# Optimization experiments

Hardware: AMD Instinct MI355X
Metric: run time of the kernel (lower is better)

## Reference

```python
import jax, jax.numpy as jnp
import numpy as np

B, DIM, W = 16, 128, 16384
HEADS, DIM_HEAD = 4, 32
HIDDEN = HEADS * DIM_HEAD  # 128
SCALE = DIM_HEAD ** -0.5
EPS = 1e-5


def setup_inputs() -> dict:
    key = jax.random.key(0)
    k0, k1, k2, k3 = jax.random.split(key, 4)
    x = jax.random.normal(k0, (B, DIM, W), dtype=jnp.float32)
    # pointwise Conv1d weights (kernel_size=1) stored as [out_ch, in_ch]
    W_qkv = jax.random.normal(k1, (HIDDEN * 3, DIM), dtype=jnp.float32) * 0.02
    W_out = jax.random.normal(k2, (DIM, HIDDEN), dtype=jnp.float32) * 0.02
    b_out = jnp.zeros((DIM,), dtype=jnp.float32)
    gamma = jnp.ones((DIM,), dtype=jnp.float32)
    beta = jnp.zeros((DIM,), dtype=jnp.float32)
    return {"x": x, "W_qkv": W_qkv, "W_out": W_out, "b_out": b_out,
            "gamma": gamma, "beta": beta}


def reference(x, W_qkv, W_out, b_out, gamma, beta):
    b, c, w = x.shape
    # pointwise conv = channel matmul: (3*hidden, c) @ (b, c, w) -> (b, 3*hidden, w)
    qkv = jnp.einsum('oc,bcw->bow', W_qkv, x)
    q, k, v = jnp.split(qkv, 3, axis=1)
    rs = lambda t: t.reshape(b, HEADS, DIM_HEAD, w)  # b (h d) w -> b h d w
    q, k, v = rs(q), rs(k), rs(v)
    q = jax.nn.softmax(q, axis=-2) * SCALE   # softmax over head-dim d
    k = jax.nn.softmax(k, axis=-1)           # softmax over length n
    v = v / w
    # context: (b h d e) = sum_n k[b h d n] v[b h e n]
    context = jnp.einsum('bhdn,bhen->bhde', k, v)
    out = jnp.einsum('bhde,bhdn->bhen', context, q)  # (b h e n)
    out = out.reshape(b, HIDDEN, w)
    y = jnp.einsum('oc,bcw->bow', W_out, out) + b_out[None, :, None]
    # channel-wise LayerNorm over dim=1 (biased variance)
    mean = jnp.mean(y, axis=1, keepdims=True)
    var = jnp.var(y, axis=1, keepdims=True)
    y = (y - mean) * jax.lax.rsqrt(var + EPS)
    return y * gamma[None, :, None] + beta[None, :, None]
```

## Files before the change

### kernel.cpp

```cpp
#include <hip/hip_runtime.h>
#include <cstddef>

#define WLEN 16384
#define SCALEQ 0.17677669529663687f
#define CB_SCALE 16777216.0f
#define CB_INV   5.9604644775390625e-08f

typedef _Float16 half8 __attribute__((ext_vector_type(8)));
typedef _Float16 half4 __attribute__((ext_vector_type(4)));
typedef float float4v __attribute__((ext_vector_type(4)));

#define WS_CTX 0
#define WS_DEN 65536
#define WS_WH  67584
#define WS_CB  92160

#define MFMA16(a, b, c) __builtin_amdgcn_mfma_f32_16x16x32_f16(a, b, c, 0, 0, 0)

__global__ __launch_bounds__(256) void k0_prep(const float* __restrict__ Wqkv,
                                               float* __restrict__ ws) {
  int idx = blockIdx.x * 256 + threadIdx.x;
  _Float16* Wh = (_Float16*)(ws + WS_WH);
  if (idx < 49152) Wh[idx] = (_Float16)Wqkv[idx];
}

__global__ __launch_bounds__(256, 2) void ka_ctx(
    const float* __restrict__ x, float* __restrict__ ws) {
  __shared__ __align__(16) _Float16 xh[64 * 136];
  __shared__ __align__(16) _Float16 ekl[4][32 * 72];
  __shared__ __align__(16) _Float16 vl[4][32 * 72];
  const int tid = threadIdx.x;
  const int lane = tid & 63, wv = tid >> 6;
  const int l15 = lane & 15, quad = lane >> 4;
  const int b = blockIdx.y, chunk = blockIdx.x;
  const _Float16* Wh = (const _Float16*)(ws + WS_WH);
  float* ctx = ws + WS_CTX;
  float* den = ws + WS_DEN;
  const float* xb = x + (size_t)b * 128 * WLEN;

  half8 bw[4][4];
  #pragma unroll
  for (int nt = 0; nt < 4; ++nt) {
    int row = (nt < 2) ? (128 + 32 * wv + nt * 16 + l15)
                       : (256 + 32 * wv + (nt - 2) * 16 + l15);
    #pragma unroll
    for (int ks = 0; ks < 4; ++ks)
      bw[nt][ks] = *(const half8*)(Wh + row * 128 + ks * 32 + quad * 8);
  }

  const float4v zero4 = {0.f, 0.f, 0.f, 0.f};
  float4v ctxa[2][2] = {zero4, zero4, zero4, zero4};
  float denr[2] = {0.f, 0.f};
  const int f = tid & 7, cq = tid >> 3;

  for (int s = 0; s < 8; ++s) {
    const int n0 = chunk * 512 + s * 64;
    __syncthreads();
    #pragma unroll
    for (int it = 0; it < 2; ++it) {
      const int nn = it * 32 + 4 * f;
      const float* p = xb + (size_t)(4 * cq) * WLEN + n0 + nn;
      float4 r0 = *(const float4*)(p);
      float4 r1 = *(const float4*)(p + WLEN);
      float4 r2 = *(const float4*)(p + 2 * WLEN);
      float4 r3 = *(const float4*)(p + 3 * WLEN);
      float c0[4] = {r0.x, r0.y, r0.z, r0.w};
      float c1[4] = {r1.x, r1.y, r1.z, r1.w};
      float c2[4] = {r2.x, r2.y, r2.z, r2.w};
      float c3[4] = {r3.x, r3.y, r3.z, r3.w};
      #pragma unroll
      for (int i = 0; i < 4; ++i) {
        half4 h;
        h[0] = (_Float16)c0[i]; h[1] = (_Float16)c1[i];
        h[2] = (_Float16)c2[i]; h[3] = (_Float16)c3[i];
        *(half4*)&xh[(nn + i) * 136 + 4 * cq] = h;
      }
    }
    __syncthreads();
    float4v acc[4][4] = {zero4, zero4, zero4, zero4, zero4, zero4, zero4, zero4,
                         zero4, zero4, zero4, zero4, zero4, zero4, zero4, zero4};
    #pragma unroll
    for (int ks = 0; ks < 4; ++ks) {
      half8 af[4];
      #pragma unroll
      for (int mt = 0; mt < 4; ++mt)
        af[mt] = *(const half8*)&xh[(mt * 16 + l15) * 136 + ks * 32 + quad * 8];
      #pragma unroll
      for (int mt = 0; mt < 4; ++mt)
        #pragma unroll
        for (int nt = 0; nt < 4; ++nt)
          acc[mt][nt] = MFMA16(af[mt], bw[nt][ks], acc[mt][nt]);
    }
    #pragma unroll
    for (int nt = 0; nt < 2; ++nt)
      #pragma unroll
      for (int mt = 0; mt < 4; ++mt) {
        half4 h;
        #pragma unroll
        for (int r = 0; r < 4; ++r) {
          float e = __expf(acc[mt][nt][r]);
          denr[nt] += e;
          h[r] = (_Float16)e;
        }
        *(half4*)&ekl[wv][(nt * 16 + l15) * 72 + mt * 16 + quad * 4] = h;
      }
    #pragma unroll
    for (int et = 0; et < 2; ++et)
      #pragma unroll
      for (int mt = 0; mt < 4; ++mt) {
        half4 h;
        #pragma unroll
        for (int r = 0; r < 4; ++r) h[r] = (_Float16)acc[mt][et + 2][r];
        *(half4*)&vl[wv][(et * 16 + l15) * 72 + mt * 16 + quad * 4] = h;
      }
    #pragma unroll
    for (int ks = 0; ks < 2; ++ks) {
      half8 ae[2], bv[2];
      #pragma unroll
      for (int dt = 0; dt < 2; ++dt)
        ae[dt] = *(const half8*)&ekl[wv][(dt * 16 + l15) * 72 + ks * 32 + quad * 8];
      #pragma unroll
      for (int et = 0; et < 2; ++et)
        bv[et] = *(const half8*)&vl[wv][(et * 16 + l15) * 72 + ks * 32 + quad * 8];
      #pragma unroll
      for (int dt = 0; dt < 2; ++dt)
        #pragma unroll
        for (int et = 0; et < 2; ++et)
          ctxa[dt][et] = MFMA16(ae[dt], bv[et], ctxa[dt][et]);
    }
  }
  #pragma unroll
  for (int dt = 0; dt < 2; ++dt)
    #pragma unroll
    for (int et = 0; et < 2; ++et)
      #pragma unroll
      for (int r = 0; r < 4; ++r)
        atomicAdd(&ctx[((b * 4 + wv) * 32 + dt * 16 + quad * 4 + r) * 32 +
                       et * 16 + l15],
                  ctxa[dt][et][r]);
  #pragma unroll
  for (int nt = 0; nt < 2; ++nt) {
    float v = denr[nt];
    v += __shfl_xor(v, 16, 64);
    v += __shfl_xor(v, 32, 64);
    if (quad == 0) atomicAdd(&den[(b * 4 + wv) * 32 + nt * 16 + l15], v);
  }
}

__global__ __launch_bounds__(256) void kb_cb(
    const float* __restrict__ Wout, float* __restrict__ ws) {
  __shared__ __align__(16) float nc[4096];
  const int b = blockIdx.x, tid = threadIdx.x;
  const float* ctx = ws + WS_CTX;
  const float* den = ws + WS_DEN;
  _Float16* cb = (_Float16*)(ws + WS_CB) + b * 16384;
  for (int i = tid; i < 4096; i += 256)
    nc[i] = ctx[b * 4096 + i] / (den[b * 128 + (i >> 5)] * 16384.0f);
  __syncthreads();
  const int o = tid >> 1, dh = (tid & 1) * 16;
  for (int h = 0; h < 4; ++h) {
    float wrow[32];
    #pragma unroll
    for (int e4 = 0; e4 < 8; ++e4) {
      float4 w4 = *(const float4*)(Wout + o * 128 + h * 32 + e4 * 4);
      wrow[e4 * 4 + 0] = w4.x; wrow[e4 * 4 + 1] = w4.y;
      wrow[e4 * 4 + 2] = w4.z; wrow[e4 * 4 + 3] = w4.w;
    }
    for (int d = 0; d < 16; ++d) {
      const float* ncr = &nc[(h * 32 + dh + d) * 32];
      float acc = 0.f;
      #pragma unroll
      for (int e = 0; e < 32; ++e) acc += wrow[e] * ncr[e];
      cb[o * 128 + h * 32 + dh + d] = (_Float16)(acc * CB_SCALE);
    }
  }
}

__global__ __launch_bounds__(256, 2) void kc_out(
    const float* __restrict__ x, const float* __restrict__ wsc,
    const float* __restrict__ b_out, const float* __restrict__ gamma,
    const float* __restrict__ beta, float* __restrict__ out) {
  __shared__ __align__(16) _Float16 xh[128 * 136];
  const int tid = threadIdx.x;
  const int lane = tid & 63, wv = tid >> 6;
  const int l15 = lane & 15, quad = lane >> 4;
  const int b = blockIdx.y, tile = blockIdx.x;
  const int n0 = tile * 128;
  const _Float16* Wh = (const _Float16*)(wsc + WS_WH);
  const _Float16* cbg = (const _Float16*)(wsc + WS_CB) + b * 16384;
  const float* xb = x + (size_t)b * 128 * WLEN;
  const float4v zero4 = {0.f, 0.f, 0.f, 0.f};

  half8 a1[2][4];
  #pragma unroll
  for (int mt = 0; mt < 2; ++mt)
    #pragma unroll
    for (int ks = 0; ks < 4; ++ks)
      a1[mt][ks] = *(const half8*)(Wh + (32 * wv + mt * 16 + l15) * 128 +
                                   ks * 32 + quad * 8);

  const int f = tid & 7, cq = tid >> 3;
  #pragma unroll
  for (int it = 0; it < 4; ++it) {
    const int nn = it * 32 + 4 * f;
    const float* p = xb + (size_t)(4 * cq) * WLEN + n0 + nn;
    float4 r0 = *(const float4*)(p);
    float4 r1 = *(const float4*)(p + WLEN);
    float4 r2 = *(const float4*)(p + 2 * WLEN);
    float4 r3 = *(const float4*)(p + 3 * WLEN);
    float c0[4] = {r0.x, r0.y, r0.z, r0.w};
    float c1[4] = {r1.x, r1.y, r1.z, r1.w};
    float c2[4] = {r2.x, r2.y, r2.z, r2.w};
    float c3[4] = {r3.x, r3.y, r3.z, r3.w};
    #pragma unroll
    for (int i = 0; i < 4; ++i) {
      half4 h;
      h[0] = (_Float16)c0[i]; h[1] = (_Float16)c1[i];
      h[2] = (_Float16)c2[i]; h[3] = (_Float16)c3[i];
      *(half4*)&xh[(nn + i) * 136 + 4 * cq] = h;
    }
  }
  __syncthreads();

  float4v acc[2][8] = {zero4, zero4, zero4, zero4, zero4, zero4, zero4, zero4,
                       zero4, zero4, zero4, zero4, zero4, zero4, zero4, zero4};
  #pragma unroll
  for (int ks = 0; ks < 4; ++ks) {
    half8 bf[8];
    #pragma unroll
    for (int nt = 0; nt < 8; ++nt)
      bf[nt] = *(const half8*)&xh[(nt * 16 + l15) * 136 + ks * 32 + quad * 8];
    #pragma unroll
    for (int mt = 0; mt < 2; ++mt)
      #pragma unroll
      for (int nt = 0; nt < 8; ++nt)
        acc[mt][nt] = MFMA16(a1[mt][ks], bf[nt], acc[mt][nt]);
  }
  #pragma unroll
  for (int nt = 0; nt < 8; ++nt) {
    float mx = -1e30f;
    #pragma unroll
    for (int mt = 0; mt < 2; ++mt)
      #pragma unroll
      for (int r = 0; r < 4; ++r) mx = fmaxf(mx, acc[mt][nt][r]);
    mx = fmaxf(mx, __shfl_xor(mx, 16, 64));
    mx = fmaxf(mx, __shfl_xor(mx, 32, 64));
    float sm = 0.f;
    #pragma unroll
    for (int mt = 0; mt < 2; ++mt)
      #pragma unroll
      for (int r = 0; r < 4; ++r) {
        float e = __expf(acc[mt][nt][r] - mx);
        acc[mt][nt][r] = e;
        sm += e;
      }
    sm += __shfl_xor(sm, 16, 64);
    sm += __shfl_xor(sm, 32, 64);
    float sc = SCALEQ / sm;
    #pragma unroll
    for (int mt = 0; mt < 2; ++mt)
      #pragma unroll
      for (int r = 0; r < 4; ++r) acc[mt][nt][r] *= sc;
  }
  __syncthreads();
  #pragma unroll
  for (int mt = 0; mt < 2; ++mt)
    #pragma unroll
    for (int nt = 0; nt < 8; ++nt) {
      half4 hq;
      #pragma unroll
      for (int r = 0; r < 4; ++r) hq[r] = (_Float16)acc[mt][nt][r];
      *(half4*)&xh[(nt * 16 + l15) * 136 + 32 * wv + mt * 16 + quad * 4] = hq;
    }
  __syncthreads();

  float4v acc2[2][8] = {zero4, zero4, zero4, zero4, zero4, zero4, zero4, zero4,
                        zero4, zero4, zero4, zero4, zero4, zero4, zero4, zero4};
  #pragma unroll
  for (int ks = 0; ks < 4; ++ks) {
    half8 aq[2];
    #pragma unroll
    for (int mt = 0; mt < 2; ++mt)
      aq[mt] = *(const half8*)&xh[(32 * wv + mt * 16 + l15) * 136 +
                                  ks * 32 + quad * 8];
    half8 bc[8];
    #pragma unroll
    for (int nt = 0; nt < 8; ++nt)
      bc[nt] = *(const half8*)(cbg + (nt * 16 + l15) * 128 + ks * 32 + quad * 8);
    #pragma unroll
    for (int mt = 0; mt < 2; ++mt)
      #pragma unroll
      for (int nt = 0; nt < 8; ++nt)
        acc2[mt][nt] = MFMA16(aq[mt], bc[nt], acc2[mt][nt]);
  }

  float bo[8], ga[8], be[8];
  #pragma unroll
  for (int nt = 0; nt < 8; ++nt) {
    int o = nt * 16 + l15;
    bo[nt] = b_out[o];
    ga[nt] = gamma[o];
    be[nt] = beta[o];
  }
  #pragma unroll
  for (int mt = 0; mt < 2; ++mt)
    #pragma unroll
    for (int nt = 0; nt < 8; ++nt)
      #pragma unroll
      for (int r = 0; r < 4; ++r)
        acc2[mt][nt][r] = acc2[mt][nt][r] * CB_INV + bo[nt];
  float meanr[2][4], invr[2][4];
  #pragma unroll
  for (int mt = 0; mt < 2; ++mt)
    #pragma unroll
    for (int r = 0; r < 4; ++r) {
      float ps = 0.f, pq = 0.f;
      #pragma unroll
      for (int nt = 0; nt < 8; ++nt) {
        float v = acc2[mt][nt][r];
        ps += v;
        pq += v * v;
      }
      ps += __shfl_xor(ps, 1, 64); pq += __shfl_xor(pq, 1, 64);
      ps += __shfl_xor(ps, 2, 64); pq += __shfl_xor(pq, 2, 64);
      ps += __shfl_xor(ps, 4, 64); pq += __shfl_xor(pq, 4, 64);
      ps += __shfl_xor(ps, 8, 64); pq += __shfl_xor(pq, 8, 64);
      float mean = ps * (1.0f / 128.0f);
      float var = pq * (1.0f / 128.0f) - mean * mean;
      meanr[mt][r] = mean;
      invr[mt][r] = rsqrtf(var + 1e-5f);
    }
  float* ob = out + (size_t)b * 128 * WLEN + n0;
  #pragma unroll
  for (int mt = 0; mt < 2; ++mt)
    #pragma unroll
    for (int nt = 0; nt < 8; ++nt) {
      float4 o4;
      o4.x = (acc2[mt][nt][0] - meanr[mt][0]) * invr[mt][0] * ga[nt] + be[nt];
      o4.y = (acc2[mt][nt][1] - meanr[mt][1]) * invr[mt][1] * ga[nt] + be[nt];
      o4.z = (acc2[mt][nt][2] - meanr[mt][2]) * invr[mt][2] * ga[nt] + be[nt];
      o4.w = (acc2[mt][nt][3] - meanr[mt][3]) * invr[mt][3] * ga[nt] + be[nt];
      *(float4*)(ob + (size_t)(nt * 16 + l15) * WLEN + 32 * wv + mt * 16 +
                 quad * 4) = o4;
    }
}

extern "C" void kernel_launch(void* const* d_in, const int* in_sizes, int n_in,
                              void* d_out, int out_size, void* d_ws, size_t ws_size,
                              hipStream_t stream) {
  const float* x    = (const float*)d_in[0];
  const float* Wqkv = (const float*)d_in[1];
  const float* Wout = (const float*)d_in[2];
  const float* bo   = (const float*)d_in[3];
  const float* gam  = (const float*)d_in[4];
  const float* bet  = (const float*)d_in[5];
  float* out = (float*)d_out;
  float* ws  = (float*)d_ws;

  hipMemsetAsync(ws, 0, (65536 + 2048) * sizeof(float), stream);
  hipLaunchKernelGGL(k0_prep, dim3(192), dim3(256), 0, stream, Wqkv, ws);
  hipLaunchKernelGGL(ka_ctx, dim3(32, 16), dim3(256), 0, stream, x, ws);
  hipLaunchKernelGGL(kb_cb, dim3(16), dim3(256), 0, stream, Wout, ws);
  hipLaunchKernelGGL(kc_out, dim3(128, 16), dim3(256), 0, stream,
                     x, ws, bo, gam, bet, out);
}
```

Measured before the change: 332.5 us.

## Double-buffer and register-prefetch x tiles in context kernel, prefetch cb in output kernel

The context kernel now processes 32-column sub-tiles with a double-buffered shared-memory tile. The next tile's global loads are prefetched into registers while the current one is computed, which cuts one barrier per step. Grid size doubles to 64 chunks and launch bounds are raised to 3 blocks per CU, with smaller LDS buffers. The output kernel software-pipelines the global loads of the combined weight matrix across the k-steps. Register pressure rises and there are twice as many atomic adds into the context accumulator.

```diff
diff --git a/kernel.cpp b/kernel.cpp
--- a/kernel.cpp
+++ b/kernel.cpp
@@ -24,11 +24,11 @@
   if (idx < 49152) Wh[idx] = (_Float16)Wqkv[idx];
 }
 
-__global__ __launch_bounds__(256, 2) void ka_ctx(
+__global__ __launch_bounds__(256, 3) void ka_ctx(
     const float* __restrict__ x, float* __restrict__ ws) {
-  __shared__ __align__(16) _Float16 xh[64 * 136];
-  __shared__ __align__(16) _Float16 ekl[4][32 * 72];
-  __shared__ __align__(16) _Float16 vl[4][32 * 72];
+  __shared__ __align__(16) _Float16 xh[2][32 * 136];
+  __shared__ __align__(16) _Float16 ekl[4][32 * 40];
+  __shared__ __align__(16) _Float16 vl[4][32 * 40];
   const int tid = threadIdx.x;
   const int lane = tid & 63, wv = tid >> 6;
   const int l15 = lane & 15, quad = lane >> 4;
@@ -52,49 +52,48 @@
   float4v ctxa[2][2] = {zero4, zero4, zero4, zero4};
   float denr[2] = {0.f, 0.f};
   const int f = tid & 7, cq = tid >> 3;
+  const float* pbase = xb + (size_t)(4 * cq) * WLEN + chunk * 256 + 4 * f;
+
+  float4 pf[4];
+  #pragma unroll
+  for (int j = 0; j < 4; ++j)
+    pf[j] = *(const float4*)(pbase + (size_t)j * WLEN);
 
   for (int s = 0; s < 8; ++s) {
-    const int n0 = chunk * 512 + s * 64;
+    _Float16* xcur = xh[s & 1];
+    float pc[4][4] = {{pf[0].x, pf[0].y, pf[0].z, pf[0].w},
+                      {pf[1].x, pf[1].y, pf[1].z, pf[1].w},
+                      {pf[2].x, pf[2].y, pf[2].z, pf[2].w},
+                      {pf[3].x, pf[3].y, pf[3].z, pf[3].w}};
+    #pragma unroll
+    for (int i = 0; i < 4; ++i) {
+      half4 h;
+      h[0] = (_Float16)pc[0][i]; h[1] = (_Float16)pc[1][i];
+      h[2] = (_Float16)pc[2][i]; h[3] = (_Float16)pc[3][i];
+      *(half4*)&xcur[(4 * f + i) * 136 + 4 * cq] = h;
+    }
+    if (s < 7) {
+      #pragma unroll
+      for (int j = 0; j < 4; ++j)
+        pf[j] = *(const float4*)(pbase + (size_t)j * WLEN + (s + 1) * 32);
+    }
     __syncthreads();
-    #pragma unroll
-    for (int it = 0; it < 2; ++it) {
-      const int nn = it * 32 + 4 * f;
-      const float* p = xb + (size_t)(4 * cq) * WLEN + n0 + nn;
-      float4 r0 = *(const float4*)(p);
-      float4 r1 = *(const float4*)(p + WLEN);
-      float4 r2 = *(const float4*)(p + 2 * WLEN);
-      float4 r3 = *(const float4*)(p + 3 * WLEN);
-      float c0[4] = {r0.x, r0.y, r0.z, r0.w};
-      float c1[4] = {r1.x, r1.y, r1.z, r1.w};
-      float c2[4] = {r2.x, r2.y, r2.z, r2.w};
-      float c3[4] = {r3.x, r3.y, r3.z, r3.w};
-      #pragma unroll
-      for (int i = 0; i < 4; ++i) {
-        half4 h;
-        h[0] = (_Float16)c0[i]; h[1] = (_Float16)c1[i];
-        h[2] = (_Float16)c2[i]; h[3] = (_Float16)c3[i];
-        *(half4*)&xh[(nn + i) * 136 + 4 * cq] = h;
-      }
-    }
-    __syncthreads();
-    float4v acc[4][4] = {zero4, zero4, zero4, zero4, zero4, zero4, zero4, zero4,
-                         zero4, zero4, zero4, zero4, zero4, zero4, zero4, zero4};
+    float4v acc[2][4] = {zero4, zero4, zero4, zero4,
+                         zero4, zero4, zero4, zero4};
     #pragma unroll
     for (int ks = 0; ks < 4; ++ks) {
-      half8 af[4];
-      #pragma unroll
-      for (int mt = 0; mt < 4; ++mt)
-        af[mt] = *(const half8*)&xh[(mt * 16 + l15) * 136 + ks * 32 + quad * 8];
-      #pragma unroll
-      for (int mt = 0; mt < 4; ++mt)
-        #pragma unroll
-        for (int nt = 0; nt < 4; ++nt)
-          acc[mt][nt] = MFMA16(af[mt], bw[nt][ks], acc[mt][nt]);
+      half8 a0 = *(const half8*)&xcur[l15 * 136 + ks * 32 + quad * 8];
+      half8 a1 = *(const half8*)&xcur[(16 + l15) * 136 + ks * 32 + quad * 8];
+      #pragma unroll
+      for (int nt = 0; nt < 4; ++nt) {
+        acc[0][nt] = MFMA16(a0, bw[nt][ks], acc[0][nt]);
+        acc[1][nt] = MFMA16(a1, bw[nt][ks], acc[1][nt]);
+      }
     }
     #pragma unroll
     for (int nt = 0; nt < 2; ++nt)
       #pragma unroll
-      for (int mt = 0; mt < 4; ++mt) {
+      for (int mt = 0; mt < 2; ++mt) {
         half4 h;
         #pragma unroll
         for (int r = 0; r < 4; ++r) {
@@ -102,32 +101,25 @@
           denr[nt] += e;
           h[r] = (_Float16)e;
         }
-        *(half4*)&ekl[wv][(nt * 16 + l15) * 72 + mt * 16 + quad * 4] = h;
+        *(half4*)&ekl[wv][(nt * 16 + l15) * 40 + mt * 16 + quad * 4] = h;
       }
     #pragma unroll
     for (int et = 0; et < 2; ++et)
       #pragma unroll
-      for (int mt = 0; mt < 4; ++mt) {
+      for (int mt = 0; mt < 2; ++mt) {
         half4 h;
         #pragma unroll
         for (int r = 0; r < 4; ++r) h[r] = (_Float16)acc[mt][et + 2][r];
-        *(half4*)&vl[wv][(et * 16 + l15) * 72 + mt * 16 + quad * 4] = h;
-      }
-    #pragma unroll
-    for (int ks = 0; ks < 2; ++ks) {
-      half8 ae[2], bv[2];
-      #pragma unroll
-      for (int dt = 0; dt < 2; ++dt)
-        ae[dt] = *(const half8*)&ekl[wv][(dt * 16 + l15) * 72 + ks * 32 + quad * 8];
-      #pragma unroll
-      for (int et = 0; et < 2; ++et)
-        bv[et] = *(const half8*)&vl[wv][(et * 16 + l15) * 72 + ks * 32 + quad * 8];
-      #pragma unroll
-      for (int dt = 0; dt < 2; ++dt)
-        #pragma unroll
-        for (int et = 0; et < 2; ++et)
-          ctxa[dt][et] = MFMA16(ae[dt], bv[et], ctxa[dt][et]);
-    }
+        *(half4*)&vl[wv][(et * 16 + l15) * 40 + mt * 16 + quad * 4] = h;
+      }
+    half8 ae0 = *(const half8*)&ekl[wv][l15 * 40 + quad * 8];
+    half8 ae1 = *(const half8*)&ekl[wv][(16 + l15) * 40 + quad * 8];
+    half8 bv0 = *(const half8*)&vl[wv][l15 * 40 + quad * 8];
+    half8 bv1 = *(const half8*)&vl[wv][(16 + l15) * 40 + quad * 8];
+    ctxa[0][0] = MFMA16(ae0, bv0, ctxa[0][0]);
+    ctxa[0][1] = MFMA16(ae0, bv1, ctxa[0][1]);
+    ctxa[1][0] = MFMA16(ae1, bv0, ctxa[1][0]);
+    ctxa[1][1] = MFMA16(ae1, bv1, ctxa[1][1]);
   }
   #pragma unroll
   for (int dt = 0; dt < 2; ++dt)
@@ -272,26 +264,34 @@
       for (int r = 0; r < 4; ++r) hq[r] = (_Float16)acc[mt][nt][r];
       *(half4*)&xh[(nt * 16 + l15) * 136 + 32 * wv + mt * 16 + quad * 4] = hq;
     }
+  half8 bc[8];
+  #pragma unroll
+  for (int nt = 0; nt < 8; ++nt)
+    bc[nt] = *(const half8*)(cbg + (nt * 16 + l15) * 128 + quad * 8);
   __syncthreads();
 
   float4v acc2[2][8] = {zero4, zero4, zero4, zero4, zero4, zero4, zero4, zero4,
                         zero4, zero4, zero4, zero4, zero4, zero4, zero4, zero4};
   #pragma unroll
   for (int ks = 0; ks < 4; ++ks) {
-    half8 aq[2];
-    #pragma unroll
-    for (int mt = 0; mt < 2; ++mt)
-      aq[mt] = *(const half8*)&xh[(32 * wv + mt * 16 + l15) * 136 +
-                                  ks * 32 + quad * 8];
-    half8 bc[8];
-    #pragma unroll
-    for (int nt = 0; nt < 8; ++nt)
-      bc[nt] = *(const half8*)(cbg + (nt * 16 + l15) * 128 + ks * 32 + quad * 8);
-    #pragma unroll
-    for (int mt = 0; mt < 2; ++mt)
+    half8 aq0 = *(const half8*)&xh[(32 * wv + l15) * 136 + ks * 32 + quad * 8];
+    half8 aq1 = *(const half8*)&xh[(32 * wv + 16 + l15) * 136 + ks * 32 + quad * 8];
+    half8 bcn[8];
+    if (ks < 3) {
       #pragma unroll
       for (int nt = 0; nt < 8; ++nt)
-        acc2[mt][nt] = MFMA16(aq[mt], bc[nt], acc2[mt][nt]);
+        bcn[nt] = *(const half8*)(cbg + (nt * 16 + l15) * 128 + (ks + 1) * 32 +
+                                  quad * 8);
+    }
+    #pragma unroll
+    for (int nt = 0; nt < 8; ++nt) {
+      acc2[0][nt] = MFMA16(aq0, bc[nt], acc2[0][nt]);
+      acc2[1][nt] = MFMA16(aq1, bc[nt], acc2[1][nt]);
+    }
+    if (ks < 3) {
+      #pragma unroll
+      for (int nt = 0; nt < 8; ++nt) bc[nt] = bcn[nt];
+    }
   }
 
   float bo[8], ga[8], be[8];
@@ -359,7 +359,7 @@
 
   hipMemsetAsync(ws, 0, (65536 + 2048) * sizeof(float), stream);
   hipLaunchKernelGGL(k0_prep, dim3(192), dim3(256), 0, stream, Wqkv, ws);
-  hipLaunchKernelGGL(ka_ctx, dim3(32, 16), dim3(256), 0, stream, x, ws);
+  hipLaunchKernelGGL(ka_ctx, dim3(64, 16), dim3(256), 0, stream, x, ws);
   hipLaunchKernelGGL(kb_cb, dim3(16), dim3(256), 0, stream, Wout, ws);
   hipLaunchKernelGGL(kc_out, dim3(128, 16), dim3(256), 0, stream,
                      x, ws, bo, gam, bet, out);
```

Result: slower. 341.7 us (+2.8%).
